# Kernel optimization log

Measured on AMD Instinct MI355X. Metric: run time of the kernel, lower is better.

Reference implementation:

```python
import jax, jax.numpy as jnp
import numpy as np

B, S, H = 2, 1024, 2048
NH, NKV, HD = 16, 8, 128
N_REP = NH // NKV
EPS = 1e-6
ROPE_THETA = 1000000.0


def act_quant(x):
    # per-token int8 absmax quantization (BitNet)
    scale = 127.0 / jnp.clip(jnp.max(jnp.abs(x), axis=-1, keepdims=True), 1e-5, None)
    return jnp.clip(jnp.round(x * scale), -128.0, 127.0) / scale


def weight_quant(w):
    # ternary weight quantization via mean absmax (BitNet 1.58b)
    scale = 1.0 / jnp.clip(jnp.mean(jnp.abs(w)), 1e-5, None)
    return jnp.clip(jnp.round(w * scale), -1.0, 1.0) / scale


def bitlinear(x, w):
    # straight-through estimator: forward quantized, backward identity
    xq = x + jax.lax.stop_gradient(act_quant(x) - x)
    wq = w + jax.lax.stop_gradient(weight_quant(w) - w)
    return xq @ wq.T


def rmsnorm(x, weight):
    return weight * (x * jax.lax.rsqrt(jnp.mean(x * x, axis=-1, keepdims=True) + EPS))


def rotate_half(x):
    h = x.shape[-1] // 2
    return jnp.concatenate([-x[..., h:], x[..., :h]], axis=-1)


def setup_inputs() -> dict:
    key = jax.random.key(0)
    ks = jax.random.split(key, 6)
    x = jax.random.normal(ks[0], (B, S, H), jnp.float32)
    wq = jax.random.normal(ks[1], (NH * HD, H), jnp.float32) * 0.02
    wk = jax.random.normal(ks[2], (NKV * HD, H), jnp.float32) * 0.02
    wv = jax.random.normal(ks[3], (NKV * HD, H), jnp.float32) * 0.02
    wo = jax.random.normal(ks[4], (H, NH * HD), jnp.float32) * 0.02
    qn = jnp.ones((HD,), jnp.float32)
    kn = jnp.ones((HD,), jnp.float32)
    # real RoPE tables: [S, HD]
    inv_freq = 1.0 / (ROPE_THETA ** (jnp.arange(0, HD, 2, dtype=jnp.float32) / HD))
    freqs = jnp.outer(jnp.arange(S, dtype=jnp.float32), inv_freq)
    emb = jnp.concatenate([freqs, freqs], axis=-1)
    return dict(x=x, cos=jnp.cos(emb), sin=jnp.sin(emb),
                wq=wq, wk=wk, wv=wv, wo=wo, qn=qn, kn=kn)


def reference(x, cos, sin, wq, wk, wv, wo, qn, kn):
    b, s, _ = x.shape
    q = bitlinear(x, wq).reshape(b, s, NH, HD)
    k = bitlinear(x, wk).reshape(b, s, NKV, HD)
    v = bitlinear(x, wv).reshape(b, s, NKV, HD)
    # per-head QK RMSNorm
    q = rmsnorm(q, qn)
    k = rmsnorm(k, kn)
    # RoPE: cos/sin [S, HD] -> unsqueeze head dim -> [S, 1, HD]
    c = cos[:, None, :]
    sn = sin[:, None, :]
    q = q * c + rotate_half(q) * sn
    k = k * c + rotate_half(k) * sn
    # GQA expand: [b,s,NKV,HD] -> [b,s,NH,HD], adjacent copies per kv head
    k = jnp.repeat(k, N_REP, axis=2)
    v = jnp.repeat(v, N_REP, axis=2)
    # to [b, h, s, d]
    q = q.transpose(0, 2, 1, 3)
    k = k.transpose(0, 2, 1, 3)
    v = v.transpose(0, 2, 1, 3)
    scores = jnp.einsum('bhqd,bhkd->bhqk', q, k) / np.float32(np.sqrt(HD))
    causal = jnp.tril(jnp.ones((s, s), bool))
    scores = jnp.where(causal, scores, jnp.finfo(scores.dtype).min)
    probs = jax.nn.softmax(scores, axis=-1)
    out = jnp.einsum('bhqk,bhkd->bhqd', probs, v)
    out = out.transpose(0, 2, 1, 3).reshape(b, s, NH * HD)
    return bitlinear(out, wo)
```

## Files before the change

### kernel.cpp

```cpp
#include <hip/hip_runtime.h>
#include <hip/hip_bf16.h>

#define TT   2048
#define HH   2048
#define SEQ  1024
#define NHQ  16
#define NKVH 8
#define HDD  128

typedef __attribute__((ext_vector_type(8))) short short8;
typedef __attribute__((ext_vector_type(4))) float f32x4;
typedef __attribute__((ext_vector_type(4))) int int4v;
typedef _Float16 half8 __attribute__((ext_vector_type(8)));

static __device__ __forceinline__ unsigned short f2h(float f) {
  union { _Float16 h; unsigned short u; } c;
  c.h = (_Float16)f;
  return c.u;
}
static __device__ __forceinline__ half8 s2h(short8 v) {
  union { short8 s; half8 h; } c;
  c.s = v;
  return c.h;
}

#define GLD_LDS16(gp, lp)                                                        \
  __builtin_amdgcn_global_load_lds(                                              \
      (const __attribute__((address_space(1))) void*)(const void*)(gp),          \
      (__attribute__((address_space(3))) void*)(void*)(lp), 16, 0, 0)

__global__ __launch_bounds__(256) void k_quant_stats(const float* __restrict__ x,
                                                     signed char* __restrict__ xq,
                                                     float* __restrict__ as_inv,
                                                     const float* __restrict__ wq,
                                                     const float* __restrict__ wk,
                                                     const float* __restrict__ wv,
                                                     const float* __restrict__ wo,
                                                     double* __restrict__ part) {
  int tid = threadIdx.x;
  int wave = tid >> 6, lane = tid & 63;
  __shared__ double redd[256];
  __shared__ float wred[4];

  if (blockIdx.x < 2048) {
    int row = blockIdx.x;
    const float4* xr4 = (const float4*)(x + (size_t)row * HH);
    float4 a = xr4[tid * 2], b = xr4[tid * 2 + 1];
    float am = fmaxf(fmaxf(fmaxf(fabsf(a.x), fabsf(a.y)), fmaxf(fabsf(a.z), fabsf(a.w))),
                     fmaxf(fmaxf(fabsf(b.x), fabsf(b.y)), fmaxf(fabsf(b.z), fabsf(b.w))));
#pragma unroll
    for (int o = 32; o; o >>= 1) am = fmaxf(am, __shfl_xor(am, o));
    if (lane == 0) wred[wave] = am;
    __syncthreads();
    am = fmaxf(fmaxf(wred[0], wred[1]), fmaxf(wred[2], wred[3]));
    am = fmaxf(am, 1e-5f);
    if (tid == 0) as_inv[row] = am / 127.f;
    float scale = 127.f / am;
    float vals[8] = {a.x, a.y, a.z, a.w, b.x, b.y, b.z, b.w};
    unsigned int u0 = 0, u1 = 0;
#pragma unroll
    for (int j = 0; j < 4; ++j) {
      int q = (int)fminf(fmaxf(rintf(vals[j] * scale), -128.f), 127.f);
      u0 |= (unsigned int)(q & 255) << (8 * j);
    }
#pragma unroll
    for (int j = 0; j < 4; ++j) {
      int q = (int)fminf(fmaxf(rintf(vals[4 + j] * scale), -128.f), 127.f);
      u1 |= (unsigned int)(q & 255) << (8 * j);
    }
    uint2 uu; uu.x = u0; uu.y = u1;
    ((uint2*)(xq + (size_t)row * HH))[tid] = uu;
  } else {
    int idx = blockIdx.x - 2048;
    int wid = idx >> 8, sub = idx & 255;
    const float* w = (wid == 0) ? wq : (wid == 1) ? wk : (wid == 2) ? wv : wo;
    int nq = ((wid == 0 || wid == 3) ? 4194304 : 2097152) >> 2;
    double s = 0.0;
    for (int i = sub * 256 + tid; i < nq; i += 256 * 256) {
      float4 v = ((const float4*)w)[i];
      s += (double)fabsf(v.x) + (double)fabsf(v.y) + (double)fabsf(v.z) + (double)fabsf(v.w);
    }
    redd[tid] = s;
    __syncthreads();
    for (int st = 128; st > 0; st >>= 1) {
      if (tid < st) redd[tid] += redd[tid + st];
      __syncthreads();
    }
    if (tid == 0) part[wid * 256 + sub] = redd[0];
  }
}

__global__ __launch_bounds__(256) void k_wquant_all(const float* __restrict__ wq,
                                                    const float* __restrict__ wk,
                                                    const float* __restrict__ wv,
                                                    signed char* __restrict__ wqk,
                                                    signed char* __restrict__ wvt,
                                                    const double* __restrict__ part,
                                                    float* __restrict__ wsc) {
  int tid = threadIdx.x;
  int wave = tid >> 6, lane = tid & 63;
  __shared__ double wred[4][4];
  __shared__ float s_wsc[4];
  const double nvals[4] = {4194304.0, 2097152.0, 2097152.0, 4194304.0};
#pragma unroll
  for (int w = 0; w < 4; ++w) {
    double s = part[w * 256 + tid];
#pragma unroll
    for (int o = 32; o; o >>= 1) s += __shfl_xor(s, o);
    if (lane == 0) wred[w][wave] = s;
  }
  __syncthreads();
  if (tid < 4) {
    double s = (wred[tid][0] + wred[tid][1]) + (wred[tid][2] + wred[tid][3]);
    float v = fmaxf((float)(s / nvals[tid]), 1e-5f);
    s_wsc[tid] = v;
    if (blockIdx.x == 0) wsc[tid] = v;
  }
  __syncthreads();
  float inv0 = 1.f / s_wsc[0], inv1 = 1.f / s_wsc[1], inv2 = 1.f / s_wsc[2];

  const int NQ = 2097152;
  for (int qi = blockIdx.x * 256 + tid; qi < NQ; qi += gridDim.x * 256) {
    const float* src; signed char* dst; float inv; int off;
    if (qi < 1048576)      { src = wq; dst = wqk;           off = qi;           inv = inv0; }
    else if (qi < 1572864) { src = wk; dst = wqk + 4194304; off = qi - 1048576; inv = inv1; }
    else                   { src = wv; dst = wvt;           off = qi - 1572864; inv = inv2; }
    float4 v = ((const float4*)src)[off];
    unsigned int u = 0;
    float vv[4] = {v.x, v.y, v.z, v.w};
#pragma unroll
    for (int j = 0; j < 4; ++j) {
      int q = (int)fminf(fmaxf(rintf(vv[j] * inv), -1.f), 1.f);
      u |= (unsigned int)(q & 255) << (8 * j);
    }
    ((unsigned int*)dst)[off] = u;
  }
}

__global__ __launch_bounds__(256) void k_gemm_i8(const signed char* __restrict__ A0,
                                                 const signed char* __restrict__ B0,
                                                 const signed char* __restrict__ B1,
                                                 unsigned short* __restrict__ dh,
                                                 const float* __restrict__ asx,
                                                 const float* __restrict__ wsc,
                                                 const float* __restrict__ qn,
                                                 const float* __restrict__ kn,
                                                 const float* __restrict__ cs,
                                                 const float* __restrict__ sn,
                                                 unsigned short* __restrict__ qf,
                                                 unsigned short* __restrict__ kf) {
  const int K = HH;
  __shared__ signed char As[2][16384];
  __shared__ signed char Bs[2][16384];
  int tid = threadIdx.x;
  int wave = tid >> 6, lane = tid & 63, l15 = lane & 15, g = lane >> 4;
  int wm = wave >> 1, wn = wave & 1;

  int gid = (blockIdx.x & 7) * 64 + (blockIdx.x >> 3);
  const signed char *Ap, *Bp;
  int bm, bn, mode;
  if (gid < 384) { mode = 0; bm = (gid / 24) * 128; bn = (gid % 24) * 128; Ap = A0; Bp = B0; }
  else { mode = 1; int vid = gid - 384; bm = (vid >> 4) * 128; bn = (vid & 15) * 128; Ap = B1; Bp = A0; }

#define GSTAGE(K0, BUF)                                                               \
  {                                                                                   \
    _Pragma("unroll")                                                                 \
    for (int r = 0; r < 4; ++r) {                                                     \
      int c = r * 256 + tid;                                                          \
      int row = c >> 3;                                                               \
      int kk2 = ((c & 7) << 4) ^ ((row & 7) << 4);                                    \
      GLD_LDS16(Ap + (size_t)(bm + row) * K + (K0) + kk2, As[BUF] + c * 16);          \
      GLD_LDS16(Bp + (size_t)(bn + row) * K + (K0) + kk2, Bs[BUF] + c * 16);          \
    }                                                                                 \
  }

  int4v acc[4][4] = {};
  GSTAGE(0, 0);
  asm volatile("s_waitcnt vmcnt(0)" ::: "memory");
  __builtin_amdgcn_s_barrier();
  __builtin_amdgcn_sched_barrier(0);

  int buf = 0;
  for (int k0 = 0; k0 < K; k0 += 128) {
    bool more = (k0 + 128 < K);
    if (more) GSTAGE(k0 + 128, buf ^ 1);
#pragma unroll
    for (int ks = 0; ks < 2; ++ks) {
      int4v af[4], bf[4];
#pragma unroll
      for (int i = 0; i < 4; ++i) {
        int ra = wm * 64 + i * 16 + l15;
        af[i] = *(const int4v*)&As[buf][ra * 128 + ((ks * 64 + g * 16) ^ ((ra & 7) << 4))];
        int rb = (mode == 0) ? (wn * 32 + (i & 1) * 16 + (i >> 1) * 64 + l15)
                             : (wn * 64 + i * 16 + l15);
        bf[i] = *(const int4v*)&Bs[buf][rb * 128 + ((ks * 64 + g * 16) ^ ((rb & 7) << 4))];
      }
      __builtin_amdgcn_s_setprio(1);
#pragma unroll
      for (int mi = 0; mi < 4; ++mi)
#pragma unroll
        for (int ni = 0; ni < 4; ++ni)
          acc[mi][ni] = __builtin_amdgcn_mfma_i32_16x16x64_i8(af[mi], bf[ni], acc[mi][ni], 0, 0, 0);
      __builtin_amdgcn_s_setprio(0);
    }
    asm volatile("s_waitcnt vmcnt(0)" ::: "memory");
    __builtin_amdgcn_s_barrier();
    __builtin_amdgcn_sched_barrier(0);
    buf ^= 1;
  }
#undef GSTAGE

  if (mode == 0) {
    bool isq = (bn < 2048);
    int hh = isq ? (bn >> 7) : ((bn - 2048) >> 7);
    float wN = isq ? wsc[0] : wsc[1];
    float ps = isq ? 0.12751743075f : 1.0f;
    const float* nw = isq ? qn : kn;
    unsigned short* oh = isq ? qf : kf;
    int nhp = isq ? NHQ : NKVH;
    float* S = (float*)&As[0][0];
    __syncthreads();
#pragma unroll
    for (int mi = 0; mi < 4; ++mi) {
#pragma unroll
      for (int rr = 0; rr < 4; ++rr) {
        int tok = bm + wm * 64 + mi * 16 + 4 * g + rr;
        float rs = asx[tok] * wN;
        float ssum = 0.f;
#pragma unroll
        for (int ni = 0; ni < 4; ++ni) {
          float v = (float)acc[mi][ni][rr] * rs;
          ssum += v * v;
        }
        ssum += __shfl_xor(ssum, 1); ssum += __shfl_xor(ssum, 2);
        ssum += __shfl_xor(ssum, 4); ssum += __shfl_xor(ssum, 8);
        if (l15 == 0) S[wn * 128 + wm * 64 + mi * 16 + 4 * g + rr] = ssum;
      }
    }
    __syncthreads();
#pragma unroll
    for (int mi = 0; mi < 4; ++mi) {
#pragma unroll
      for (int rr = 0; rr < 4; ++rr) {
        int rloc = wm * 64 + mi * 16 + 4 * g + rr;
        int tok = bm + rloc;
        float rs = asx[tok] * wN;
        float inv = rsqrtf((S[rloc] + S[128 + rloc]) * (1.f / 128.f) + 1e-6f);
        int s = tok & (SEQ - 1);
        float nv[4];
#pragma unroll
        for (int ni = 0; ni < 4; ++ni) {
          int d = wn * 32 + (ni & 1) * 16 + (ni >> 1) * 64 + l15;
          nv[ni] = nw[d] * ((float)acc[mi][ni][rr] * rs) * inv;
        }
#pragma unroll
        for (int ni = 0; ni < 4; ++ni) {
          int d = wn * 32 + (ni & 1) * 16 + (ni >> 1) * 64 + l15;
          float oo = nv[ni ^ 2];
          float rh = (ni < 2) ? -oo : oo;
          float res = (nv[ni] * cs[s * 128 + d] + rh * sn[s * 128 + d]) * ps;
          size_t oi = ((size_t)tok * nhp + hh) * 128 + d;
          oh[oi] = f2h(res);
        }
      }
    }
  } else {
    float w2 = wsc[2];
#pragma unroll
    for (int mi = 0; mi < 4; ++mi) {
#pragma unroll
      for (int rr = 0; rr < 4; ++rr) {
        int crow = bm + wm * 64 + mi * 16 + 4 * g + rr;
#pragma unroll
        for (int ni = 0; ni < 4; ++ni) {
          int ccol = bn + wn * 64 + ni * 16 + l15;
          float v = (float)acc[mi][ni][rr] * asx[ccol] * w2;
          size_t ad = ((size_t)((ccol >> 10) * 1024 + crow)) * 1024 + (ccol & 1023);
          dh[ad] = f2h(v);
        }
      }
    }
  }
}

__global__ __launch_bounds__(256) void k_gemm_o(const signed char* __restrict__ A,
                                                const signed char* __restrict__ B,
                                                float* __restrict__ d0,
                                                const float* __restrict__ asx,
                                                const float* __restrict__ wsc) {
  const int K = HH;
  __shared__ signed char As[2][16384];
  __shared__ signed char Bs[2][8192];
  int tid = threadIdx.x;
  int wave = tid >> 6, lane = tid & 63, l15 = lane & 15, g = lane >> 4;
  int gid = (blockIdx.x & 7) * 64 + (blockIdx.x >> 3);
  int bm = (gid >> 5) * 128, bn = (gid & 31) * 64;

#define OSTAGE(K0, BUF)                                                               \
  {                                                                                   \
    _Pragma("unroll")                                                                 \
    for (int r = 0; r < 4; ++r) {                                                     \
      int c = r * 256 + tid;                                                          \
      int row = c >> 3;                                                               \
      int kk2 = ((c & 7) << 4) ^ ((row & 7) << 4);                                    \
      GLD_LDS16(A + (size_t)(bm + row) * K + (K0) + kk2, As[BUF] + c * 16);           \
    }                                                                                 \
    _Pragma("unroll")                                                                 \
    for (int r = 0; r < 2; ++r) {                                                     \
      int c = r * 256 + tid;                                                          \
      int row = c >> 3;                                                               \
      int kk2 = ((c & 7) << 4) ^ ((row & 7) << 4);                                    \
      GLD_LDS16(B + (size_t)(bn + row) * K + (K0) + kk2, Bs[BUF] + c * 16);           \
    }                                                                                 \
  }

  int4v acc[2][4] = {};
  OSTAGE(0, 0);
  asm volatile("s_waitcnt vmcnt(0)" ::: "memory");
  __builtin_amdgcn_s_barrier();
  __builtin_amdgcn_sched_barrier(0);

  int buf = 0;
  for (int k0 = 0; k0 < K; k0 += 128) {
    bool more = (k0 + 128 < K);
    if (more) OSTAGE(k0 + 128, buf ^ 1);
#pragma unroll
    for (int ks = 0; ks < 2; ++ks) {
      int4v af[2], bf[4];
#pragma unroll
      for (int i = 0; i < 2; ++i) {
        int ra = wave * 32 + i * 16 + l15;
        af[i] = *(const int4v*)&As[buf][ra * 128 + ((ks * 64 + g * 16) ^ ((ra & 7) << 4))];
      }
#pragma unroll
      for (int n = 0; n < 4; ++n) {
        int rb = n * 16 + l15;
        bf[n] = *(const int4v*)&Bs[buf][rb * 128 + ((ks * 64 + g * 16) ^ ((rb & 7) << 4))];
      }
      __builtin_amdgcn_s_setprio(1);
#pragma unroll
      for (int mi = 0; mi < 2; ++mi)
#pragma unroll
        for (int ni = 0; ni < 4; ++ni)
          acc[mi][ni] = __builtin_amdgcn_mfma_i32_16x16x64_i8(af[mi], bf[ni], acc[mi][ni], 0, 0, 0);
      __builtin_amdgcn_s_setprio(0);
    }
    asm volatile("s_waitcnt vmcnt(0)" ::: "memory");
    __builtin_amdgcn_s_barrier();
    __builtin_amdgcn_sched_barrier(0);
    buf ^= 1;
  }
#undef OSTAGE

  float w3 = wsc[3];
#pragma unroll
  for (int mi = 0; mi < 2; ++mi) {
#pragma unroll
    for (int rr = 0; rr < 4; ++rr) {
      int crow = bm + wave * 32 + mi * 16 + 4 * g + rr;
      float rs = asx[crow] * w3;
#pragma unroll
      for (int ni = 0; ni < 4; ++ni) {
        int ccol = bn + ni * 16 + l15;
        d0[(size_t)crow * 2048 + ccol] = (float)acc[ni == 0 ? mi : mi][ni][rr] * rs;
      }
    }
  }
}

__global__ __launch_bounds__(256) void k_actquant(const float* __restrict__ x,
                                                  signed char* __restrict__ xq,
                                                  float* __restrict__ as_inv) {
  int row = blockIdx.x, tid = threadIdx.x;
  int wave = tid >> 6, lane = tid & 63;
  const float4* xr4 = (const float4*)(x + (size_t)row * HH);
  float4 a = xr4[tid * 2], b = xr4[tid * 2 + 1];
  float am = fmaxf(fmaxf(fmaxf(fabsf(a.x), fabsf(a.y)), fmaxf(fabsf(a.z), fabsf(a.w))),
                   fmaxf(fmaxf(fabsf(b.x), fabsf(b.y)), fmaxf(fabsf(b.z), fabsf(b.w))));
#pragma unroll
  for (int o = 32; o; o >>= 1) am = fmaxf(am, __shfl_xor(am, o));
  __shared__ float wred[4];
  if (lane == 0) wred[wave] = am;
  __syncthreads();
  am = fmaxf(fmaxf(wred[0], wred[1]), fmaxf(wred[2], wred[3]));
  am = fmaxf(am, 1e-5f);
  if (tid == 0) as_inv[row] = am / 127.f;
  float scale = 127.f / am;
  float vals[8] = {a.x, a.y, a.z, a.w, b.x, b.y, b.z, b.w};
  unsigned int u0 = 0, u1 = 0;
#pragma unroll
  for (int j = 0; j < 4; ++j) {
    int q = (int)fminf(fmaxf(rintf(vals[j] * scale), -128.f), 127.f);
    u0 |= (unsigned int)(q & 255) << (8 * j);
  }
#pragma unroll
  for (int j = 0; j < 4; ++j) {
    int q = (int)fminf(fmaxf(rintf(vals[4 + j] * scale), -128.f), 127.f);
    u1 |= (unsigned int)(q & 255) << (8 * j);
  }
  uint2 uu; uu.x = u0; uu.y = u1;
  ((uint2*)(xq + (size_t)row * HH))[tid] = uu;
}

__global__ __launch_bounds__(256) void k_attn_mfma(const unsigned short* __restrict__ qfp,
                                                   const unsigned short* __restrict__ kfp,
                                                   const unsigned short* __restrict__ vfp,
                                                   float* __restrict__ o,
                                                   const float* __restrict__ wsc,
                                                   const float* __restrict__ wo_f32,
                                                   signed char* __restrict__ wot) {
  int tid = threadIdx.x;
  if (blockIdx.x >= 512) {
    int bx = blockIdx.x - 512;
    float inv = 1.f / wsc[3];
    for (int qi = bx * 256 + tid; qi < 1048576; qi += 128 * 256) {
      float4 v = ((const float4*)wo_f32)[qi];
      unsigned int u = 0;
      float vv[4] = {v.x, v.y, v.z, v.w};
#pragma unroll
      for (int j = 0; j < 4; ++j) {
        int q = (int)fminf(fmaxf(rintf(vv[j] * inv), -1.f), 1.f);
        u |= (unsigned int)(q & 255) << (8 * j);
      }
      ((unsigned int*)wot)[qi] = u;
    }
    return;
  }

  int chunk = blockIdx.x & 7, j = blockIdx.x >> 3;
  int qt, yyi;
  if (j < 32) { qt = 15 - (j >> 2); yyi = j & 3; }
  else        { qt = (j - 32) >> 2; yyi = (j - 32) & 3; }
  int yy = (chunk << 2) + yyi;
  int b = yy >> 4, h = yy & 15, kvh = h >> 1;
  int wave = tid >> 6, lane = tid & 63;
  int l15 = lane & 15, g = lane >> 4;
  int q0w = qt * 64 + wave * 16;
  int qglob = q0w + l15;

  __shared__ unsigned short Kf[2][8192];
  __shared__ unsigned short Vf[2][8192];
  __shared__ unsigned short Plds[4][16][72];

  half8 qf[4];
  {
    const unsigned short* qb = qfp + ((size_t)(b * SEQ + qglob) * NHQ + h) * HDD + g * 8;
#pragma unroll
    for (int c = 0; c < 4; ++c) qf[c] = s2h(*(const short8*)(qb + c * 32));
  }
  half8 vones;
#pragma unroll
  for (int c = 0; c < 8; ++c) vones[c] = (_Float16)1.0f;

#define STAGE64(KV0N, BUF)                                                            \
  {                                                                                   \
    _Pragma("unroll")                                                                 \
    for (int tch = 0; tch < 4; ++tch) {                                               \
      int c = tch * 256 + tid;                                                        \
      int ki = c >> 4, jb = (c & 15) << 4;                                            \
      int js = jb ^ ((ki & 7) << 4);                                                  \
      size_t kbase = ((size_t)(b * SEQ + (KV0N) + ki) * NKVH + kvh) * HDD;            \
      GLD_LDS16((const char*)(kfp + kbase) + js, &Kf[BUF][c * 8]);                    \
      int d = c >> 3, jv = (c & 7) << 4;                                              \
      int jvs = jv ^ ((d & 7) << 4);                                                  \
      size_t vbase = ((size_t)(b * 1024 + kvh * 128 + d)) * SEQ + (KV0N);             \
      GLD_LDS16((const char*)(vfp + vbase) + jvs, &Vf[BUF][c * 8]);                   \
    }                                                                                 \
  }

  f32x4 acc[9] = {};
  float m_run = -INFINITY;
  int nkv = qt + 1;

  STAGE64(0, 0);
  asm volatile("s_waitcnt vmcnt(0) lgkmcnt(0)" ::: "memory");
  __builtin_amdgcn_s_barrier();
  __builtin_amdgcn_sched_barrier(0);

  int buf = 0;
  for (int kv = 0; kv < nkv; ++kv) {
    int kv0 = kv * 64;
    bool more = (kv + 1 < nkv);
    if (more) STAGE64(kv0 + 64, buf ^ 1);
    bool active = (kv0 <= q0w + 15);
    if (active) {
      const char* Kb = (const char*)&Kf[buf][0];
      const char* Vb = (const char*)&Vf[buf][0];
      float sc[4][4];
      __builtin_amdgcn_s_setprio(1);
#pragma unroll
      for (int t = 0; t < 4; ++t) {
        int row = 16 * t + l15;
        int rbyte = row * 256, sw = (row & 7) << 4;
        f32x4 s = {0.f, 0.f, 0.f, 0.f};
#pragma unroll
        for (int c = 0; c < 4; ++c) {
          int off = rbyte + ((c * 64 + g * 16) ^ sw);
          half8 kf8 = s2h(*(const short8*)(Kb + off));
          s = __builtin_amdgcn_mfma_f32_16x16x32_f16(kf8, qf[c], s, 0, 0, 0);
        }
#pragma unroll
        for (int r = 0; r < 4; ++r) sc[t][r] = s[r];
      }
      __builtin_amdgcn_s_setprio(0);
      if (kv0 + 63 > q0w) {
#pragma unroll
        for (int t = 0; t < 4; ++t)
#pragma unroll
          for (int r = 0; r < 4; ++r)
            if (kv0 + 16 * t + 4 * g + r > qglob) sc[t][r] = -INFINITY;
      }
      float pmax = -INFINITY;
#pragma unroll
      for (int t = 0; t < 4; ++t)
#pragma unroll
        for (int r = 0; r < 4; ++r) pmax = fmaxf(pmax, sc[t][r]);
      if (!__all(pmax <= m_run + 10.f)) {
        pmax = fmaxf(pmax, __shfl_xor(pmax, 16));
        pmax = fmaxf(pmax, __shfl_xor(pmax, 32));
        float mnew = fmaxf(m_run, pmax);
        float corr = exp2f(m_run - mnew);
        m_run = mnew;
        float corro[4];
#pragma unroll
        for (int r = 0; r < 4; ++r) corro[r] = __shfl(corr, 4 * g + r);
#pragma unroll
        for (int dt = 0; dt < 9; ++dt)
#pragma unroll
          for (int r = 0; r < 4; ++r) acc[dt][r] *= corro[r];
      }
      ushort4 wh;
#pragma unroll
      for (int t = 0; t < 4; ++t) {
        wh.x = f2h(exp2f(sc[t][0] - m_run));
        wh.y = f2h(exp2f(sc[t][1] - m_run));
        wh.z = f2h(exp2f(sc[t][2] - m_run));
        wh.w = f2h(exp2f(sc[t][3] - m_run));
        *(ushort4*)&Plds[wave][l15][16 * t + 4 * g] = wh;
      }
      half8 pa0 = s2h(*(const short8*)&Plds[wave][l15][8 * g]);
      half8 pa1 = s2h(*(const short8*)&Plds[wave][l15][32 + 8 * g]);
      __builtin_amdgcn_s_setprio(1);
#pragma unroll
      for (int dt = 0; dt < 8; ++dt) {
        int d = dt * 16 + l15;
        int rbase = d * 128, sw = (d & 7) << 4;
        half8 v0 = s2h(*(const short8*)(Vb + rbase + ((g * 16) ^ sw)));
        half8 v1 = s2h(*(const short8*)(Vb + rbase + ((64 + g * 16) ^ sw)));
        acc[dt] = __builtin_amdgcn_mfma_f32_16x16x32_f16(pa0, v0, acc[dt], 0, 0, 0);
        acc[dt] = __builtin_amdgcn_mfma_f32_16x16x32_f16(pa1, v1, acc[dt], 0, 0, 0);
      }
      acc[8] = __builtin_amdgcn_mfma_f32_16x16x32_f16(pa0, vones, acc[8], 0, 0, 0);
      acc[8] = __builtin_amdgcn_mfma_f32_16x16x32_f16(pa1, vones, acc[8], 0, 0, 0);
      __builtin_amdgcn_s_setprio(0);
    }
    asm volatile("s_waitcnt vmcnt(0)" ::: "memory");
    __builtin_amdgcn_s_barrier();
    __builtin_amdgcn_sched_barrier(0);
    buf ^= 1;
  }
#undef STAGE64

  float linv[4];
#pragma unroll
  for (int r = 0; r < 4; ++r) linv[r] = 1.f / acc[8][r];
#pragma unroll
  for (int r = 0; r < 4; ++r) {
    size_t orow = ((size_t)(b * SEQ + q0w + 4 * g + r) * NHQ + h) * HDD + l15;
#pragma unroll
    for (int dt = 0; dt < 8; ++dt)
      o[orow + dt * 16] = acc[dt][r] * linv[r];
  }
}

extern "C" void kernel_launch(void* const* d_in, const int* in_sizes, int n_in,
                              void* d_out, int out_size, void* d_ws, size_t ws_size,
                              hipStream_t stream) {
  const float* x  = (const float*)d_in[0];
  const float* cs = (const float*)d_in[1];
  const float* sn = (const float*)d_in[2];
  const float* wq = (const float*)d_in[3];
  const float* wk = (const float*)d_in[4];
  const float* wv = (const float*)d_in[5];
  const float* wo = (const float*)d_in[6];
  const float* qn = (const float*)d_in[7];
  const float* kn = (const float*)d_in[8];
  float* out = (float*)d_out;
  char* ws = (char*)d_ws;

  const size_t MB = 1024 * 1024;
  size_t o_xq  = 0;
  size_t o_wqk = 4  * MB;
  size_t o_wvt = 10 * MB;
  size_t o_wot = 12 * MB;
  size_t o_vt  = 16 * MB;
  size_t o_qf  = 20 * MB;
  size_t o_kf  = 28 * MB;
  size_t o_ao  = 32 * MB;
  size_t o_aq  = 48 * MB;
  size_t o_as  = 52 * MB;
  size_t o_as2 = o_as  + 8192;
  size_t o_prt = o_as2 + 8192;
  size_t o_wsc = o_prt + 8192;

  signed char* xq  = (signed char*)(ws + o_xq);
  signed char* wqk = (signed char*)(ws + o_wqk);
  signed char* wvt = (signed char*)(ws + o_wvt);
  signed char* wot = (signed char*)(ws + o_wot);
  unsigned short* vt = (unsigned short*)(ws + o_vt);
  unsigned short* qf = (unsigned short*)(ws + o_qf);
  unsigned short* kf = (unsigned short*)(ws + o_kf);
  float* ao = (float*)(ws + o_ao);
  signed char* aq = (signed char*)(ws + o_aq);
  float* asx = (float*)(ws + o_as);
  float* as2 = (float*)(ws + o_as2);
  double* prt = (double*)(ws + o_prt);
  float* wsc = (float*)(ws + o_wsc);

  k_quant_stats<<<3072, 256, 0, stream>>>(x, xq, asx, wq, wk, wv, wo, prt);

  k_wquant_all<<<1024, 256, 0, stream>>>(wq, wk, wv, wqk, wvt, prt, wsc);

  k_gemm_i8<<<512, 256, 0, stream>>>(xq, wqk, wvt, vt, asx, wsc,
                                     qn, kn, cs, sn, qf, kf);

  k_attn_mfma<<<640, 256, 0, stream>>>(qf, kf, vt, ao, wsc, wo, wot);

  k_actquant<<<TT, 256, 0, stream>>>(ao, aq, as2);
  k_gemm_o<<<512, 256, 0, stream>>>(aq, wot, out, as2, wsc);
}
```

Baseline: 108.6 us.

## Pair high and low causal query tiles per attention block, 32 rows per wave

Each attention block now handles two query tiles, one from the heavy end of the causal triangle and one from the light end. Waves 0-1 take the high tile and waves 2-3 the low tile, and each wave computes 32 query rows with two accumulator sets that share each K/V fragment read from LDS. The grid shrinks from 512 to 256 attention blocks, which balances causal work per block and halves K/V staging traffic per query row. In exchange, register pressure roughly doubles, occupancy may drop, the low-tile waves idle once past their causal range, and there are fewer blocks to spread across CUs. A redundant ternary index in the output GEMM is also cleaned up.

Result: slower. 119.1 us (+9.7%).

```diff
diff --git a/kernel.cpp b/kernel.cpp
--- a/kernel.cpp
+++ b/kernel.cpp
@@ -362,7 +362,7 @@
 #pragma unroll
       for (int ni = 0; ni < 4; ++ni) {
         int ccol = bn + ni * 16 + l15;
-        d0[(size_t)crow * 2048 + ccol] = (float)acc[ni == 0 ? mi : mi][ni][rr] * rs;
+        d0[(size_t)crow * 2048 + ccol] = (float)acc[mi][ni][rr] * rs;
       }
     }
   }
@@ -410,8 +410,8 @@
                                                    const float* __restrict__ wo_f32,
                                                    signed char* __restrict__ wot) {
   int tid = threadIdx.x;
-  if (blockIdx.x >= 512) {
-    int bx = blockIdx.x - 512;
+  if (blockIdx.x >= 256) {
+    int bx = blockIdx.x - 256;
     float inv = 1.f / wsc[3];
     for (int qi = bx * 256 + tid; qi < 1048576; qi += 128 * 256) {
       float4 v = ((const float4*)wo_f32)[qi];
@@ -428,25 +428,30 @@
   }
 
   int chunk = blockIdx.x & 7, j = blockIdx.x >> 3;
-  int qt, yyi;
-  if (j < 32) { qt = 15 - (j >> 2); yyi = j & 3; }
-  else        { qt = (j - 32) >> 2; yyi = (j - 32) & 3; }
-  int yy = (chunk << 2) + yyi;
+  int qpair = j >> 2;
+  int yy = (chunk << 2) + (j & 3);
   int b = yy >> 4, h = yy & 15, kvh = h >> 1;
+  int qt_h = 15 - qpair, qt_l = qpair;
   int wave = tid >> 6, lane = tid & 63;
   int l15 = lane & 15, g = lane >> 4;
-  int q0w = qt * 64 + wave * 16;
-  int qglob = q0w + l15;
+  int qt_w = (wave < 2) ? qt_h : qt_l;
+  int q0w = qt_w * 64 + (wave & 1) * 32;
+  int qg0 = q0w + l15;
+  int qg1 = q0w + 16 + l15;
 
   __shared__ unsigned short Kf[2][8192];
   __shared__ unsigned short Vf[2][8192];
-  __shared__ unsigned short Plds[4][16][72];
-
-  half8 qf[4];
+  __shared__ unsigned short Plds[4][2][16][68];
+
+  half8 qf0[4], qf1[4];
   {
-    const unsigned short* qb = qfp + ((size_t)(b * SEQ + qglob) * NHQ + h) * HDD + g * 8;
-#pragma unroll
-    for (int c = 0; c < 4; ++c) qf[c] = s2h(*(const short8*)(qb + c * 32));
+    const unsigned short* qb0 = qfp + ((size_t)(b * SEQ + qg0) * NHQ + h) * HDD + g * 8;
+    const unsigned short* qb1 = qfp + ((size_t)(b * SEQ + qg1) * NHQ + h) * HDD + g * 8;
+#pragma unroll
+    for (int c = 0; c < 4; ++c) {
+      qf0[c] = s2h(*(const short8*)(qb0 + c * 32));
+      qf1[c] = s2h(*(const short8*)(qb1 + c * 32));
+    }
   }
   half8 vones;
 #pragma unroll
@@ -468,9 +473,9 @@
     }                                                                                 \
   }
 
-  f32x4 acc[9] = {};
-  float m_run = -INFINITY;
-  int nkv = qt + 1;
+  f32x4 accA[9] = {}, accB[9] = {};
+  float m0 = -INFINITY, m1 = -INFINITY;
+  int nkv = qt_h + 1;
 
   STAGE64(0, 0);
   asm volatile("s_waitcnt vmcnt(0) lgkmcnt(0)" ::: "memory");
@@ -482,64 +487,85 @@
     int kv0 = kv * 64;
     bool more = (kv + 1 < nkv);
     if (more) STAGE64(kv0 + 64, buf ^ 1);
-    bool active = (kv0 <= q0w + 15);
+    bool active = (kv0 <= q0w + 31);
     if (active) {
       const char* Kb = (const char*)&Kf[buf][0];
       const char* Vb = (const char*)&Vf[buf][0];
-      float sc[4][4];
+      float s0[4][4], s1[4][4];
       __builtin_amdgcn_s_setprio(1);
 #pragma unroll
       for (int t = 0; t < 4; ++t) {
         int row = 16 * t + l15;
         int rbyte = row * 256, sw = (row & 7) << 4;
-        f32x4 s = {0.f, 0.f, 0.f, 0.f};
+        f32x4 a0 = {0.f, 0.f, 0.f, 0.f};
+        f32x4 a1 = {0.f, 0.f, 0.f, 0.f};
 #pragma unroll
         for (int c = 0; c < 4; ++c) {
           int off = rbyte + ((c * 64 + g * 16) ^ sw);
           half8 kf8 = s2h(*(const short8*)(Kb + off));
-          s = __builtin_amdgcn_mfma_f32_16x16x32_f16(kf8, qf[c], s, 0, 0, 0);
+          a0 = __builtin_amdgcn_mfma_f32_16x16x32_f16(kf8, qf0[c], a0, 0, 0, 0);
+          a1 = __builtin_amdgcn_mfma_f32_16x16x32_f16(kf8, qf1[c], a1, 0, 0, 0);
         }
 #pragma unroll
-        for (int r = 0; r < 4; ++r) sc[t][r] = s[r];
+        for (int r = 0; r < 4; ++r) { s0[t][r] = a0[r]; s1[t][r] = a1[r]; }
       }
       __builtin_amdgcn_s_setprio(0);
       if (kv0 + 63 > q0w) {
 #pragma unroll
         for (int t = 0; t < 4; ++t)
 #pragma unroll
-          for (int r = 0; r < 4; ++r)
-            if (kv0 + 16 * t + 4 * g + r > qglob) sc[t][r] = -INFINITY;
-      }
-      float pmax = -INFINITY;
+          for (int r = 0; r < 4; ++r) {
+            int key = kv0 + 16 * t + 4 * g + r;
+            if (key > qg0) s0[t][r] = -INFINITY;
+            if (key > qg1) s1[t][r] = -INFINITY;
+          }
+      }
+      float p0 = -INFINITY, p1 = -INFINITY;
 #pragma unroll
       for (int t = 0; t < 4; ++t)
 #pragma unroll
-        for (int r = 0; r < 4; ++r) pmax = fmaxf(pmax, sc[t][r]);
-      if (!__all(pmax <= m_run + 10.f)) {
-        pmax = fmaxf(pmax, __shfl_xor(pmax, 16));
-        pmax = fmaxf(pmax, __shfl_xor(pmax, 32));
-        float mnew = fmaxf(m_run, pmax);
-        float corr = exp2f(m_run - mnew);
-        m_run = mnew;
-        float corro[4];
-#pragma unroll
-        for (int r = 0; r < 4; ++r) corro[r] = __shfl(corr, 4 * g + r);
+        for (int r = 0; r < 4; ++r) {
+          p0 = fmaxf(p0, s0[t][r]);
+          p1 = fmaxf(p1, s1[t][r]);
+        }
+      if (!__all(p0 <= m0 + 10.f && p1 <= m1 + 10.f)) {
+        p0 = fmaxf(p0, __shfl_xor(p0, 16)); p0 = fmaxf(p0, __shfl_xor(p0, 32));
+        p1 = fmaxf(p1, __shfl_xor(p1, 16)); p1 = fmaxf(p1, __shfl_xor(p1, 32));
+        float mn0 = fmaxf(m0, p0), mn1 = fmaxf(m1, p1);
+        float c0 = exp2f(m0 - mn0), c1 = exp2f(m1 - mn1);
+        m0 = mn0; m1 = mn1;
+        float co0[4], co1[4];
+#pragma unroll
+        for (int r = 0; r < 4; ++r) {
+          co0[r] = __shfl(c0, 4 * g + r);
+          co1[r] = __shfl(c1, 4 * g + r);
+        }
 #pragma unroll
         for (int dt = 0; dt < 9; ++dt)
 #pragma unroll
-          for (int r = 0; r < 4; ++r) acc[dt][r] *= corro[r];
+          for (int r = 0; r < 4; ++r) {
+            accA[dt][r] *= co0[r];
+            accB[dt][r] *= co1[r];
+          }
       }
       ushort4 wh;
 #pragma unroll
       for (int t = 0; t < 4; ++t) {
-        wh.x = f2h(exp2f(sc[t][0] - m_run));
-        wh.y = f2h(exp2f(sc[t][1] - m_run));
-        wh.z = f2h(exp2f(sc[t][2] - m_run));
-        wh.w = f2h(exp2f(sc[t][3] - m_run));
-        *(ushort4*)&Plds[wave][l15][16 * t + 4 * g] = wh;
-      }
-      half8 pa0 = s2h(*(const short8*)&Plds[wave][l15][8 * g]);
-      half8 pa1 = s2h(*(const short8*)&Plds[wave][l15][32 + 8 * g]);
+        wh.x = f2h(exp2f(s0[t][0] - m0));
+        wh.y = f2h(exp2f(s0[t][1] - m0));
+        wh.z = f2h(exp2f(s0[t][2] - m0));
+        wh.w = f2h(exp2f(s0[t][3] - m0));
+        *(ushort4*)&Plds[wave][0][l15][16 * t + 4 * g] = wh;
+        wh.x = f2h(exp2f(s1[t][0] - m1));
+        wh.y = f2h(exp2f(s1[t][1] - m1));
+        wh.z = f2h(exp2f(s1[t][2] - m1));
+        wh.w = f2h(exp2f(s1[t][3] - m1));
+        *(ushort4*)&Plds[wave][1][l15][16 * t + 4 * g] = wh;
+      }
+      half8 pa0s0 = s2h(*(const short8*)&Plds[wave][0][l15][8 * g]);
+      half8 pa1s0 = s2h(*(const short8*)&Plds[wave][0][l15][32 + 8 * g]);
+      half8 pa0s1 = s2h(*(const short8*)&Plds[wave][1][l15][8 * g]);
+      half8 pa1s1 = s2h(*(const short8*)&Plds[wave][1][l15][32 + 8 * g]);
       __builtin_amdgcn_s_setprio(1);
 #pragma unroll
       for (int dt = 0; dt < 8; ++dt) {
@@ -547,11 +573,15 @@
         int rbase = d * 128, sw = (d & 7) << 4;
         half8 v0 = s2h(*(const short8*)(Vb + rbase + ((g * 16) ^ sw)));
         half8 v1 = s2h(*(const short8*)(Vb + rbase + ((64 + g * 16) ^ sw)));
-        acc[dt] = __builtin_amdgcn_mfma_f32_16x16x32_f16(pa0, v0, acc[dt], 0, 0, 0);
-        acc[dt] = __builtin_amdgcn_mfma_f32_16x16x32_f16(pa1, v1, acc[dt], 0, 0, 0);
-      }
-      acc[8] = __builtin_amdgcn_mfma_f32_16x16x32_f16(pa0, vones, acc[8], 0, 0, 0);
-      acc[8] = __builtin_amdgcn_mfma_f32_16x16x32_f16(pa1, vones, acc[8], 0, 0, 0);
+        accA[dt] = __builtin_amdgcn_mfma_f32_16x16x32_f16(pa0s0, v0, accA[dt], 0, 0, 0);
+        accA[dt] = __builtin_amdgcn_mfma_f32_16x16x32_f16(pa1s0, v1, accA[dt], 0, 0, 0);
+        accB[dt] = __builtin_amdgcn_mfma_f32_16x16x32_f16(pa0s1, v0, accB[dt], 0, 0, 0);
+        accB[dt] = __builtin_amdgcn_mfma_f32_16x16x32_f16(pa1s1, v1, accB[dt], 0, 0, 0);
+      }
+      accA[8] = __builtin_amdgcn_mfma_f32_16x16x32_f16(pa0s0, vones, accA[8], 0, 0, 0);
+      accA[8] = __builtin_amdgcn_mfma_f32_16x16x32_f16(pa1s0, vones, accA[8], 0, 0, 0);
+      accB[8] = __builtin_amdgcn_mfma_f32_16x16x32_f16(pa0s1, vones, accB[8], 0, 0, 0);
+      accB[8] = __builtin_amdgcn_mfma_f32_16x16x32_f16(pa1s1, vones, accB[8], 0, 0, 0);
       __builtin_amdgcn_s_setprio(0);
     }
     asm volatile("s_waitcnt vmcnt(0)" ::: "memory");
@@ -561,15 +591,21 @@
   }
 #undef STAGE64
 
-  float linv[4];
-#pragma unroll
-  for (int r = 0; r < 4; ++r) linv[r] = 1.f / acc[8][r];
+  float lA[4], lB[4];
 #pragma unroll
   for (int r = 0; r < 4; ++r) {
-    size_t orow = ((size_t)(b * SEQ + q0w + 4 * g + r) * NHQ + h) * HDD + l15;
-#pragma unroll
-    for (int dt = 0; dt < 8; ++dt)
-      o[orow + dt * 16] = acc[dt][r] * linv[r];
+    lA[r] = 1.f / accA[8][r];
+    lB[r] = 1.f / accB[8][r];
+  }
+#pragma unroll
+  for (int r = 0; r < 4; ++r) {
+    size_t orA = ((size_t)(b * SEQ + q0w + 4 * g + r) * NHQ + h) * HDD + l15;
+    size_t orB = ((size_t)(b * SEQ + q0w + 16 + 4 * g + r) * NHQ + h) * HDD + l15;
+#pragma unroll
+    for (int dt = 0; dt < 8; ++dt) {
+      o[orA + dt * 16] = accA[dt][r] * lA[r];
+      o[orB + dt * 16] = accB[dt][r] * lB[r];
+    }
   }
 }
 
@@ -624,7 +660,7 @@
   k_gemm_i8<<<512, 256, 0, stream>>>(xq, wqk, wvt, vt, asx, wsc,
                                      qn, kn, cs, sn, qf, kf);
 
-  k_attn_mfma<<<640, 256, 0, stream>>>(qf, kf, vt, ao, wsc, wo, wot);
+  k_attn_mfma<<<384, 256, 0, stream>>>(qf, kf, vt, ao, wsc, wo, wot);
 
   k_actquant<<<TT, 256, 0, stream>>>(ao, aq, as2);
   k_gemm_o<<<512, 256, 0, stream>>>(aq, wot, out, as2, wsc);
```
